# Optimization experiments

Hardware: AMD Instinct MI355X
Metric: run time of the kernel (lower is better)

## Reference

```python
import jax, jax.numpy as jnp
import numpy as np
import math

B, L, D, H = 8, 2048, 1024, 16
DK = D // H
FACTOR = 1
TOP_K = int(FACTOR * math.log(L))  # = 7


def _linear(x, W, b):
    # torch nn.Linear: y = x @ W.T + b, W shape (out, in)
    return x @ W.T + b


def setup_inputs() -> dict:
    rng = jax.random.key(0)
    ks = jax.random.split(rng, 11)
    s = 1.0 / math.sqrt(D)
    inp = {
        "query": jax.random.normal(ks[0], (B, L, D), jnp.float32),
        "key": jax.random.normal(ks[1], (B, L, D), jnp.float32),
        "value": jax.random.normal(ks[2], (B, L, D), jnp.float32),
        "Wq": jax.random.normal(ks[3], (D, D), jnp.float32) * s,
        "bq": jnp.zeros((D,), jnp.float32),
        "Wk": jax.random.normal(ks[4], (D, D), jnp.float32) * s,
        "bk": jnp.zeros((D,), jnp.float32),
        "Wv": jax.random.normal(ks[5], (D, D), jnp.float32) * s,
        "bv": jnp.zeros((D,), jnp.float32),
        "Wo": jax.random.normal(ks[6], (D, D), jnp.float32) * s,
        "bo": jnp.zeros((D,), jnp.float32),
    }
    return inp


def _autocorrelation(q, k, v):
    # q,k,v: (B, H, DK, L)
    q_fft = jnp.fft.rfft(q, axis=-1)
    k_fft = jnp.fft.rfft(k, axis=-1)
    corr = jnp.fft.irfft(q_fft * jnp.conj(k_fft), n=L, axis=-1)  # (B,H,DK,L)

    mean_value = jnp.mean(corr, axis=2)                 # (B,H,L)
    weights, index = jax.lax.top_k(mean_value, TOP_K)   # (B,H,TOP_K)
    tmp_corr = jax.nn.softmax(weights, axis=-1)         # (B,H,TOP_K)

    t = jnp.arange(L)[None, None, :]                    # (1,1,L)
    delays_agg = jnp.zeros_like(v)
    for i in range(TOP_K):  # TOP_K=7, static small loop
        # torch.roll(v, -delay, -1)[..., t] == v[..., (t+delay) % L]
        idx = (t + index[:, :, i:i + 1]) % L            # (B,H,L)
        idx = jnp.broadcast_to(idx[:, :, None, :], v.shape)
        pattern = jnp.take_along_axis(v, idx, axis=-1)  # (B,H,DK,L)
        delays_agg = delays_agg + pattern * tmp_corr[:, :, i][:, :, None, None]
    return delays_agg, tmp_corr


def reference(query, key, value, Wq, bq, Wk, bk, Wv, bv, Wo, bo):
    residual = query
    # project and split heads -> (B, H, DK, L)
    q = _linear(query, Wq, bq).reshape(B, L, H, DK).transpose(0, 2, 3, 1)
    k = _linear(key, Wk, bk).reshape(B, L, H, DK).transpose(0, 2, 3, 1)
    v = _linear(value, Wv, bv).reshape(B, L, H, DK).transpose(0, 2, 3, 1)

    agg, corr_weights = _autocorrelation(q, k, v)       # (B,H,DK,L)
    corr_value = agg.transpose(0, 3, 1, 2).reshape(B, L, D)
    corr_value = _linear(corr_value, Wo, bo)
    # dropout in eval mode = identity
    return corr_value + residual, corr_weights
```

## Files before the change

kernel.cpp:

```cpp
#include <hip/hip_runtime.h>
#include <hip/hip_bf16.h>
#include <math.h>

#define BB   8
#define LL   2048
#define DD   1024
#define HH   16
#define DKK  64
#define TOPK 7

typedef unsigned short u16;
typedef short short8 __attribute__((ext_vector_type(8)));
typedef short s4v    __attribute__((ext_vector_type(4)));
typedef float f32x4  __attribute__((ext_vector_type(4)));
typedef int   int4v  __attribute__((ext_vector_type(4)));
typedef char  char16v __attribute__((ext_vector_type(16)));

#define QT_B    0ull
#define KT_B    67108864ull
#define VBF_B   134217728ull
#define XH_B    167772160ull
#define WH_B    201326592ull
#define WL_B    203423744ull
#define PART_B  201326592ull
#define PART_STRIDE 2064
#define TOPW_B  209780736ull
#define TOPI_B  209784320ull

#define SX_INV  5461.3333f
#define SW_INV  174762.67f
#define CS1     6.8664551e-5f
#define CS2     2.6822090e-7f

__device__ __forceinline__ int2 xcd_swizzle_8x128() {
    const int lin = blockIdx.y * gridDim.x + blockIdx.x;
    const int swz = (lin & 7) * 128 + (lin >> 3);
    return make_int2(swz & 7, swz >> 3);
}

__device__ __forceinline__ u16 f2bf(float f) {
    unsigned u = __float_as_uint(f);
    unsigned r = u + 0x7FFFu + ((u >> 16) & 1u);
    return (u16)(r >> 16);
}
__device__ __forceinline__ float bf2f(u16 h) {
    return __uint_as_float((unsigned)h << 16);
}

__global__ __launch_bounds__(256) void k_split_i8(
    const float* __restrict__ x, char* __restrict__ hi, char* __restrict__ lo,
    float inv_s, int n16)
{
    for (int i = blockIdx.x * 256 + threadIdx.x; i < n16; i += gridDim.x * 256) {
        const float4* xp = (const float4*)(x + (size_t)i * 16);
        float f[16];
        #pragma unroll
        for (int v = 0; v < 4; ++v) {
            float4 t = xp[v];
            f[v*4+0] = t.x; f[v*4+1] = t.y; f[v*4+2] = t.z; f[v*4+3] = t.w;
        }
        char16v h, l;
        #pragma unroll
        for (int j = 0; j < 16; ++j) {
            int q = __float2int_rn(f[j] * inv_s);
            q = min(max(q, -32639), 32639);
            int xl = ((q + 128) & 255) - 128;
            int xh = (q - xl) >> 8;
            h[j] = (char)xh; l[j] = (char)xl;
        }
        *(char16v*)(hi + (size_t)i * 16) = h;
        *(char16v*)(lo + (size_t)i * 16) = l;
    }
}

__global__ __launch_bounds__(256) void k_cvt_bf16(
    const float* __restrict__ x, u16* __restrict__ hi, int n8)
{
    for (int i = blockIdx.x * 256 + threadIdx.x; i < n8; i += gridDim.x * 256) {
        const float4* xp = (const float4*)(x + (size_t)i * 8);
        float4 v0 = xp[0], v1 = xp[1];
        float f[8] = {v0.x, v0.y, v0.z, v0.w, v1.x, v1.y, v1.z, v1.w};
        short8 h8;
        #pragma unroll
        for (int j = 0; j < 8; ++j) h8[j] = (short)f2bf(f[j]);
        *(short8*)(hi + (size_t)i * 8) = h8;
    }
}

__global__ __launch_bounds__(256) void k_transpose_bf(
    const u16* __restrict__ src, u16* __restrict__ dst)
{
    __shared__ u16 tile[32][34];
    const int tx = threadIdx.x & 31, ty = threadIdx.x >> 5;
    const int row0 = blockIdx.y * 32;
    const int col0 = blockIdx.x * 32;
    #pragma unroll
    for (int i = 0; i < 4; ++i)
        tile[ty + i * 8][tx] = src[(size_t)(row0 + ty + i * 8) * 2048 + col0 + tx];
    __syncthreads();
    const int b  = row0 >> 10;
    const int d0 = row0 & 1023;
    #pragma unroll
    for (int i = 0; i < 4; ++i) {
        const int l = col0 + ty + i * 8;
        dst[(size_t)((b << 11) + l) * 1024 + d0 + tx] = tile[tx][ty + i * 8];
    }
}

__device__ __forceinline__ void async16(u16* l, const u16* g) {
    __builtin_amdgcn_global_load_lds(
        (const __attribute__((address_space(1))) void*)g,
        (__attribute__((address_space(3))) void*)l, 16, 0, 0);
}
__device__ __forceinline__ void async16b(char* l, const char* g) {
    __builtin_amdgcn_global_load_lds(
        (const __attribute__((address_space(1))) void*)g,
        (__attribute__((address_space(3))) void*)l, 16, 0, 0);
}

__global__ __launch_bounds__(256, 2) void gemm_i8split(
    const char* __restrict__ Ah, const char* __restrict__ Al,
    const char* __restrict__ Bh, const char* __restrict__ Bl,
    const float* __restrict__ bias, float* __restrict__ outp)
{
    __shared__ __align__(16) char lds[2][4][8192];
    const int t = threadIdx.x;
    const int w = t >> 6, lane = t & 63;
    const int2 tb = xcd_swizzle_8x128();
    const int m0 = tb.y * 128, n0 = tb.x * 128;
    const int srow = lane >> 2, sslot = lane & 3;
    const int r15 = lane & 15, kg = lane >> 4;
    const int wr = w >> 1, wc = w & 1;
    const int r4 = (lane >> 4) * 4;
    const int swzb = (kg ^ (r15 & 3)) << 4;
    const int a_off = (wr * 64 + r15) * 64 + swzb;
    const int b_off = (wc * 64 + r15) * 64 + swzb;

    int4v acc1[4][4], acc2[4][4];
    #pragma unroll
    for (int i = 0; i < 4; ++i)
        #pragma unroll
        for (int j = 0; j < 4; ++j) {
            acc1[i][j] = (int4v){0,0,0,0};
            acc2[i][j] = (int4v){0,0,0,0};
        }

    #define STAGE8(buf, kt)                                                       \
    {                                                                             \
        const int gc0 = (kt) * 64;                                                \
        _Pragma("unroll")                                                         \
        for (int i = 0; i < 2; ++i) {                                             \
            const int row  = w * 32 + i * 16 + srow;                              \
            const int kch  = (sslot ^ (row & 3)) << 4;                            \
            const int loff = w * 2048 + i * 1024;                                 \
            async16b(&lds[buf][0][loff], Ah + (size_t)(m0 + row) * 1024 + gc0 + kch); \
            async16b(&lds[buf][1][loff], Bh + (size_t)(n0 + row) * 1024 + gc0 + kch); \
            async16b(&lds[buf][2][loff], Al + (size_t)(m0 + row) * 1024 + gc0 + kch); \
            async16b(&lds[buf][3][loff], Bl + (size_t)(n0 + row) * 1024 + gc0 + kch); \
        }                                                                         \
    }

    #define COMP8(buf)                                                            \
    {                                                                             \
        const char* cb = &lds[buf][0][0];                                         \
        int4v ah[4], bh4[4], al[4], bl[4];                                        \
        _Pragma("unroll")                                                         \
        for (int mi = 0; mi < 4; ++mi) ah[mi] = *(const int4v*)(cb + a_off + mi * 1024); \
        _Pragma("unroll")                                                         \
        for (int nj = 0; nj < 4; ++nj) bh4[nj] = *(const int4v*)(cb + 8192 + b_off + nj * 1024); \
        _Pragma("unroll")                                                         \
        for (int mi = 0; mi < 4; ++mi)                                            \
            _Pragma("unroll")                                                     \
            for (int nj = 0; nj < 4; ++nj)                                        \
                acc1[mi][nj] = __builtin_amdgcn_mfma_i32_16x16x64_i8(ah[mi], bh4[nj], acc1[mi][nj], 0, 0, 0); \
        _Pragma("unroll")                                                         \
        for (int nj = 0; nj < 4; ++nj) bl[nj] = *(const int4v*)(cb + 24576 + b_off + nj * 1024); \
        _Pragma("unroll")                                                         \
        for (int mi = 0; mi < 4; ++mi)                                            \
            _Pragma("unroll")                                                     \
            for (int nj = 0; nj < 4; ++nj)                                        \
                acc2[mi][nj] = __builtin_amdgcn_mfma_i32_16x16x64_i8(ah[mi], bl[nj], acc2[mi][nj], 0, 0, 0); \
        _Pragma("unroll")                                                         \
        for (int mi = 0; mi < 4; ++mi) al[mi] = *(const int4v*)(cb + 16384 + a_off + mi * 1024); \
        _Pragma("unroll")                                                         \
        for (int mi = 0; mi < 4; ++mi)                                            \
            _Pragma("unroll")                                                     \
            for (int nj = 0; nj < 4; ++nj)                                        \
                acc2[mi][nj] = __builtin_amdgcn_mfma_i32_16x16x64_i8(al[mi], bh4[nj], acc2[mi][nj], 0, 0, 0); \
    }

    STAGE8(0, 0);
    __syncthreads();
    int cur = 0;
    for (int kt = 0; kt < 15; ++kt) {
        STAGE8(cur ^ 1, kt + 1);
        COMP8(cur);
        __syncthreads();
        cur ^= 1;
    }
    COMP8(cur);

    #pragma unroll
    for (int nj = 0; nj < 4; ++nj) {
        const int n = n0 + wc * 64 + nj * 16 + r15;
        const float bs = bias[n];
        #pragma unroll
        for (int mi = 0; mi < 4; ++mi) {
            const int m = m0 + wr * 64 + mi * 16 + r4;
            const int b = m >> 11;
            const int l = m & 2047;
            float4 v;
            v.x = fmaf(CS1, (float)acc1[mi][nj][0], fmaf(CS2, (float)acc2[mi][nj][0], bs));
            v.y = fmaf(CS1, (float)acc1[mi][nj][1], fmaf(CS2, (float)acc2[mi][nj][1], bs));
            v.z = fmaf(CS1, (float)acc1[mi][nj][2], fmaf(CS2, (float)acc2[mi][nj][2], bs));
            v.w = fmaf(CS1, (float)acc1[mi][nj][3], fmaf(CS2, (float)acc2[mi][nj][3], bs));
            *(float4*)(outp + (((size_t)((b << 10) + n)) << 11) + l) = v;
        }
    }
    #undef STAGE8
    #undef COMP8
}

template<int NPROD, int EPI>
__global__ __launch_bounds__(256, 2) void gemm_mfma_bt(
    const u16* __restrict__ Ah, const u16* __restrict__ Al,
    const u16* __restrict__ Bh, const u16* __restrict__ Bl,
    const float* __restrict__ bias, const float* __restrict__ resid,
    float* __restrict__ outp)
{
    constexpr int NARR = (NPROD == 3) ? 4 : 2;
    __shared__ __align__(16) u16 lds[2 * NARR * 4096];
    const int t = threadIdx.x;
    const int w = t >> 6, lane = t & 63;
    const int2 tb = xcd_swizzle_8x128();
    const int m0 = tb.y * 128, n0 = tb.x * 128;
    const int srow = lane >> 2, sslot = lane & 3;
    const int r15 = lane & 15, kg = lane >> 4;
    const int wr = w >> 1, wc = w & 1;
    const int r4 = (lane >> 4) * 4;
    const int swz16 = (kg ^ (r15 & 3)) << 3;
    const int a_off = ((wr * 64 + r15) << 5) + swz16;
    const int b_off = ((wc * 64 + r15) << 5) + swz16;

    f32x4 acc[4][4];
    #pragma unroll
    for (int i = 0; i < 4; ++i)
        #pragma unroll
        for (int j = 0; j < 4; ++j)
            acc[i][j] = (f32x4){0.f, 0.f, 0.f, 0.f};

    #define STAGE(buf, kt)                                                        \
    {                                                                             \
        const int k0s = (kt) * 32;                                                \
        u16* base = &lds[(buf) * NARR * 4096];                                    \
        _Pragma("unroll")                                                         \
        for (int i = 0; i < 2; ++i) {                                             \
            const int row = w * 32 + i * 16 + srow;                               \
            const int kch = ((sslot ^ (row & 3)) << 3);                           \
            const int loff = w * 1024 + i * 512;                                  \
            async16(&base[loff],            Ah + (size_t)(m0 + row) * 1024 + k0s + kch); \
            async16(&base[4096 + loff],     Bh + (size_t)(n0 + row) * 1024 + k0s + kch); \
        }                                                                         \
    }

    #define COMPUTE(buf)                                                          \
    {                                                                             \
        const u16* cb = &lds[(buf) * NARR * 4096];                                \
        short8 ah[4], bh[4];                                                      \
        _Pragma("unroll")                                                         \
        for (int mi = 0; mi < 4; ++mi) ah[mi] = *(const short8*)(cb + a_off + mi * 512); \
        _Pragma("unroll")                                                         \
        for (int nj = 0; nj < 4; ++nj) bh[nj] = *(const short8*)(cb + 4096 + b_off + nj * 512); \
        _Pragma("unroll")                                                         \
        for (int mi = 0; mi < 4; ++mi)                                            \
            _Pragma("unroll")                                                     \
            for (int nj = 0; nj < 4; ++nj)                                        \
                acc[mi][nj] = __builtin_amdgcn_mfma_f32_16x16x32_bf16(ah[mi], bh[nj], acc[mi][nj], 0, 0, 0); \
    }

    STAGE(0, 0);
    __syncthreads();
    int cur = 0;
    for (int kt = 0; kt < 31; ++kt) {
        STAGE(cur ^ 1, kt + 1);
        COMPUTE(cur);
        __syncthreads();
        cur ^= 1;
    }
    COMPUTE(cur);

    if (EPI == 0) {
        #pragma unroll
        for (int nj = 0; nj < 4; ++nj) {
            const int n = n0 + wc * 64 + nj * 16 + r15;
            const float bs = bias[n];
            #pragma unroll
            for (int mi = 0; mi < 4; ++mi) {
                const int m = m0 + wr * 64 + mi * 16 + r4;
                const int b = m >> 11;
                const int l = m & 2047;
                float4 v;
                v.x = acc[mi][nj][0] + bs;
                v.y = acc[mi][nj][1] + bs;
                v.z = acc[mi][nj][2] + bs;
                v.w = acc[mi][nj][3] + bs;
                *(float4*)(outp + (((size_t)((b << 10) + n)) << 11) + l) = v;
            }
        }
    } else if (EPI == 2) {
        u16* outb = (u16*)outp;
        #pragma unroll
        for (int nj = 0; nj < 4; ++nj) {
            const int n = n0 + wc * 64 + nj * 16 + r15;
            const float bs = bias[n];
            #pragma unroll
            for (int mi = 0; mi < 4; ++mi) {
                const int m = m0 + wr * 64 + mi * 16 + r4;
                const int b = m >> 11;
                const int l = m & 2047;
                s4v v;
                #pragma unroll
                for (int r = 0; r < 4; ++r) v[r] = (short)f2bf(acc[mi][nj][r] + bs);
                *(s4v*)(outb + (((size_t)((b << 10) + n)) << 11) + l) = v;
            }
        }
    } else {
        #pragma unroll
        for (int mi = 0; mi < 4; ++mi) {
            #pragma unroll
            for (int r = 0; r < 4; ++r) {
                const int m = m0 + wr * 64 + mi * 16 + r4 + r;
                const float* rrow = resid + ((size_t)m << 10);
                float* orow = outp + ((size_t)m << 10);
                #pragma unroll
                for (int nj = 0; nj < 4; ++nj) {
                    const int n = n0 + wc * 64 + nj * 16 + r15;
                    orow[n] = acc[mi][nj][r] + bias[n] + rrow[n];
                }
            }
        }
    }
    #undef STAGE
    #undef COMPUTE
}

#define IDX(i) ((i) + ((i) >> 3))
#define FFT_BUF 2304

__device__ __forceinline__ float2 c_add(float2 a, float2 b){ return make_float2(a.x+b.x, a.y+b.y); }
__device__ __forceinline__ float2 c_sub(float2 a, float2 b){ return make_float2(a.x-b.x, a.y-b.y); }
__device__ __forceinline__ float2 cmul(float2 a, float2 b){
    return make_float2(fmaf(a.x, b.x, -a.y*b.y), fmaf(a.x, b.y, a.y*b.x));
}
template<bool INV>
__device__ __forceinline__ float2 rot90(float2 z) {
    return INV ? make_float2(-z.y, z.x) : make_float2(z.y, -z.x);
}

template<bool INV>
__device__ __forceinline__ void dft8(const float2* a, float2* y) {
    const float r = 0.70710678118654752f;
    float2 e0 = c_add(a[0], a[4]), e1 = c_sub(a[0], a[4]);
    float2 e2 = c_add(a[2], a[6]), e3 = rot90<INV>(c_sub(a[2], a[6]));
    float2 E0 = c_add(e0, e2), E2 = c_sub(e0, e2);
    float2 E1 = c_add(e1, e3), E3 = c_sub(e1, e3);
    float2 o0 = c_add(a[1], a[5]), o1 = c_sub(a[1], a[5]);
    float2 o2 = c_add(a[3], a[7]), o3 = rot90<INV>(c_sub(a[3], a[7]));
    float2 O0 = c_add(o0, o2), O2 = c_sub(o0, o2);
    float2 O1 = c_add(o1, o3), O3 = c_sub(o1, o3);
    float2 T1 = INV ? make_float2(r*(O1.x - O1.y), r*(O1.x + O1.y))
                    : make_float2(r*(O1.x + O1.y), r*(O1.y - O1.x));
    float2 T2 = rot90<INV>(O2);
    float2 T3 = INV ? make_float2(-r*(O3.x + O3.y), r*(O3.x - O3.y))
                    : make_float2(r*(O3.y - O3.x), -r*(O3.x + O3.y));
    y[0] = c_add(E0, O0); y[4] = c_sub(E0, O0);
    y[1] = c_add(E1, T1); y[5] = c_sub(E1, T1);
    y[2] = c_add(E2, T2); y[6] = c_sub(E2, T2);
    y[3] = c_add(E3, T3); y[7] = c_sub(E3, T3);
}

template<bool INV>
__device__ float2* fft2048_r8(float2* bufA, float2* bufB, const float2* twd, int tid)
{
    float2* src = bufA;
    float2* dst = bufB;
    #pragma unroll
    for (int st = 0; st < 3; ++st) {
        const int s = 1 << (3 * st);
        const int u = tid;
        const int sp = u & ~(s - 1);
        float2 a[8], y[8];
        #pragma unroll
        for (int t = 0; t < 8; ++t) a[t] = src[IDX(u + (t << 8))];
        dft8<INV>(a, y);
        float2 w1 = twd[sp];
        if (INV) w1.y = -w1.y;
        const int ob = u + 7 * sp;
        dst[IDX(ob)]     = y[0];
        dst[IDX(ob + s)] = cmul(y[1], w1);
        float2 w = w1;
        #pragma unroll
        for (int t = 2; t < 8; ++t) {
            w = cmul(w, w1);
            dst[IDX(ob + t * s)] = cmul(y[t], w);
        }
        __syncthreads();
        float2* tmp = src; src = dst; dst = tmp;
    }
    #pragma unroll
    for (int h = 0; h < 2; ++h) {
        const int u = tid + (h << 8);
        float2 a0 = src[IDX(u)],        a1 = src[IDX(u + 512)];
        float2 a2 = src[IDX(u + 1024)], a3 = src[IDX(u + 1536)];
        float2 b0 = c_add(a0, a2), b1 = c_sub(a0, a2);
        float2 b2 = c_add(a1, a3), b3 = rot90<INV>(c_sub(a1, a3));
        dst[IDX(u)]        = c_add(b0, b2);
        dst[IDX(u + 512)]  = c_add(b1, b3);
        dst[IDX(u + 1024)] = c_sub(b0, b2);
        dst[IDX(u + 1536)] = c_sub(b1, b3);
    }
    __syncthreads();
    return dst;
}

__global__ __launch_bounds__(256) void fft_corr_partial(
    const float* __restrict__ qT, const float* __restrict__ kT,
    float* __restrict__ part)
{
    __shared__ float2 bufA[FFT_BUF];
    __shared__ float2 bufB[FFT_BUF];
    __shared__ float2 twd[256];
    const int tid = threadIdx.x;
    const int blk = blockIdx.x;
    const int bh  = blk >> 3, g = blk & 7;
    {
        float s, c;
        sincosf((float)tid * 3.0679615757712823e-3f, &s, &c);
        twd[tid] = make_float2(c, -s);
    }
    float2 racc[4];
    #pragma unroll
    for (int ii = 0; ii < 4; ++ii) racc[ii] = make_float2(0.f, 0.f);
    float2 racc4 = make_float2(0.f, 0.f);

    const float* qbase = qT + ((size_t)bh * DKK + g * 8) * LL;
    const float* kbase = kT + ((size_t)bh * DKK + g * 8) * LL;
    for (int dd = 0; dd < 8; ++dd) {
        __syncthreads();
        const float* qr = qbase + (size_t)dd * LL;
        const float* kr = kbase + (size_t)dd * LL;
        #pragma unroll
        for (int j = 0; j < 8; ++j) {
            const int l = tid + (j << 8);
            bufA[IDX(l)] = make_float2(qr[l], kr[l]);
        }
        __syncthreads();
        float2* res = fft2048_r8<false>(bufA, bufB, twd, tid);
        #pragma unroll
        for (int ii = 0; ii < 4; ++ii) {
            const int f = tid + (ii << 8);
            float2 zf = res[IDX(f)];
            float2 zc = res[IDX((2048 - f) & 2047)];
            float2 Q = make_float2(0.5f*(zf.x + zc.x), 0.5f*(zf.y - zc.y));
            float2 K = make_float2(0.5f*(zf.y + zc.y), -0.5f*(zf.x - zc.x));
            racc[ii].x += Q.x*K.x + Q.y*K.y;
            racc[ii].y += Q.y*K.x - Q.x*K.y;
        }
        if (tid == 0) {
            float2 zf = res[IDX(1024)];
            racc4.x += zf.x * zf.y;
        }
    }
    float* po = part + (size_t)blk * PART_STRIDE;
    #pragma unroll
    for (int ii = 0; ii < 4; ++ii) {
        const int f = tid + (ii << 8);
        po[2*f]     = racc[ii].x;
        po[2*f + 1] = racc[ii].y;
    }
    if (tid == 0) { po[2048] = racc4.x; po[2049] = racc4.y; }
}

__global__ __launch_bounds__(256) void fft_inv_topk(
    const float* __restrict__ part, float* __restrict__ out1,
    float* __restrict__ topw, int* __restrict__ topi)
{
    __shared__ float2 bufA[FFT_BUF];
    __shared__ float2 bufB[FFT_BUF];
    __shared__ float2 twd[256];
    __shared__ float  mv[2048];
    __shared__ float  rv[256];
    __shared__ int    ri[256];
    __shared__ float  selv[TOPK];
    __shared__ int    seli[TOPK];
    const int tid = threadIdx.x;
    const int bh  = blockIdx.x;
    {
        float s, c;
        sincosf((float)tid * 3.0679615757712823e-3f, &s, &c);
        twd[tid] = make_float2(c, -s);
    }
    for (int f = tid; f < 1025; f += 256) {
        float sx = 0.f, sy = 0.f;
        for (int g2 = 0; g2 < 8; ++g2) {
            const float* po = part + (size_t)(bh * 8 + g2) * PART_STRIDE + 2*f;
            sx += po[0]; sy += po[1];
        }
        bufA[IDX(f)] = make_float2(sx, sy);
        if (f > 0 && f < 1024) bufA[IDX(2048 - f)] = make_float2(sx, -sy);
    }
    __syncthreads();
    float2* res = fft2048_r8<true>(bufA, bufB, twd, tid);
    const float scale = 1.0f / (2048.0f * 64.0f);
    #pragma unroll
    for (int j = 0; j < 8; ++j) {
        const int l = tid + (j << 8);
        mv[l] = res[IDX(l)].x * scale;
    }
    __syncthreads();
    for (int it = 0; it < TOPK; ++it) {
        float bvv = -3.0e38f; int bii = 0;
        #pragma unroll
        for (int c = 0; c < 8; ++c) {
            const int idx = tid * 8 + c;
            const float v = mv[idx];
            if (v > bvv) { bvv = v; bii = idx; }
        }
        rv[tid] = bvv; ri[tid] = bii;
        __syncthreads();
        for (int off = 128; off > 0; off >>= 1) {
            if (tid < off) {
                const float v2 = rv[tid + off]; const int i2 = ri[tid + off];
                if (v2 > rv[tid] || (v2 == rv[tid] && i2 < ri[tid])) {
                    rv[tid] = v2; ri[tid] = i2;
                }
            }
            __syncthreads();
        }
        if (tid == 0) { selv[it] = rv[0]; seli[it] = ri[0]; mv[ri[0]] = -3.0e38f; }
        __syncthreads();
    }
    if (tid == 0) {
        const float mx = selv[0];
        float e[TOPK]; float ssum = 0.f;
        #pragma unroll
        for (int i = 0; i < TOPK; ++i) { e[i] = expf(selv[i] - mx); ssum += e[i]; }
        const float inv = 1.0f / ssum;
        #pragma unroll
        for (int i = 0; i < TOPK; ++i) {
            const float w = e[i] * inv;
            out1[bh * TOPK + i] = w;
            topw[bh * TOPK + i] = w;
            topi[bh * TOPK + i] = seli[i];
        }
    }
}

__global__ __launch_bounds__(256) void gather_agg_bf(
    const u16* __restrict__ vbf, const float* __restrict__ topw,
    const int* __restrict__ topi, u16* __restrict__ aggbf)
{
    __shared__ float vrow[2048];
    __shared__ float wv[TOPK];
    __shared__ int   wi[TOPK];
    const int blk = blockIdx.x;
    const int bh  = blk >> 6;
    const int tid = threadIdx.x;
    if (tid < TOPK) {
        wv[tid] = topw[bh * TOPK + tid];
        wi[tid] = topi[bh * TOPK + tid];
    }
    const u16* vr = vbf + (size_t)blk * LL;
    short8 v8 = *(const short8*)(vr + tid * 8);
    #pragma unroll
    for (int j = 0; j < 8; ++j) vrow[tid * 8 + j] = bf2f((u16)v8[j]);
    __syncthreads();
    u16* ar = aggbf + (size_t)blk * LL;
    short8 o8;
    #pragma unroll
    for (int j = 0; j < 8; ++j) {
        const int l = tid * 8 + j;
        float s = 0.f;
        #pragma unroll
        for (int i = 0; i < TOPK; ++i)
            s = fmaf(wv[i], vrow[(l + wi[i]) & 2047], s);
        o8[j] = (short)f2bf(s);
    }
    *(short8*)(ar + tid * 8) = o8;
}

extern "C" void kernel_launch(void* const* d_in, const int* in_sizes, int n_in,
                              void* d_out, int out_size, void* d_ws, size_t ws_size,
                              hipStream_t stream)
{
    const float* query = (const float*)d_in[0];
    const float* key   = (const float*)d_in[1];
    const float* value = (const float*)d_in[2];
    const float* Wq    = (const float*)d_in[3];
    const float* bq    = (const float*)d_in[4];
    const float* Wk    = (const float*)d_in[5];
    const float* bk    = (const float*)d_in[6];
    const float* Wv    = (const float*)d_in[7];
    const float* bv    = (const float*)d_in[8];
    const float* Wo    = (const float*)d_in[9];
    const float* bo    = (const float*)d_in[10];
    float* out = (float*)d_out;
    char*  ws  = (char*)d_ws;

    float* qT    = (float*)(ws + QT_B);
    float* kT    = (float*)(ws + KT_B);
    u16*   vbf   = (u16*)(ws + VBF_B);
    float* part  = (float*)(ws + PART_B);
    float* topw  = (float*)(ws + TOPW_B);
    int*   topi  = (int*)(ws + TOPI_B);
    char* qxh8 = (char*)(ws + KT_B);
    char* qxl8 = (char*)(ws + KT_B + 16777216ull);
    char* qwh8 = (char*)(ws + VBF_B);
    char* qwl8 = (char*)(ws + VBF_B + 1048576ull);
    char* kxh8 = (char*)(ws + VBF_B);
    char* kxl8 = (char*)(ws + VBF_B + 16777216ull);
    char* kwh8 = (char*)(ws + WH_B);
    char* kwl8 = (char*)(ws + WH_B + 1048576ull);
    u16* vxh = (u16*)(ws + XH_B);
    u16* vwh = (u16*)(ws + WH_B);
    u16* aggbf  = (u16*)(ws + XH_B);
    u16* aggrow = (u16*)(ws + VBF_B);
    u16* owh = (u16*)(ws + WH_B);

    const int NX8  = BB * LL * DD / 8;
    const int NW8  = DD * DD / 8;
    const int NX16 = BB * LL * DD / 16;
    const int NW16 = DD * DD / 16;
    dim3 gg(DD / 128, (BB * LL) / 128);

    k_split_i8<<<2048, 256, 0, stream>>>(query, qxh8, qxl8, SX_INV, NX16);
    k_split_i8<<<256, 256, 0, stream>>>(Wq, qwh8, qwl8, SW_INV, NW16);
    gemm_i8split<<<gg, 256, 0, stream>>>(qxh8, qxl8, qwh8, qwl8, bq, qT);
    k_split_i8<<<2048, 256, 0, stream>>>(key, kxh8, kxl8, SX_INV, NX16);
    k_split_i8<<<256, 256, 0, stream>>>(Wk, kwh8, kwl8, SW_INV, NW16);
    gemm_i8split<<<gg, 256, 0, stream>>>(kxh8, kxl8, kwh8, kwl8, bk, kT);
    k_cvt_bf16<<<2048, 256, 0, stream>>>(value, vxh, NX8);
    k_cvt_bf16<<<512, 256, 0, stream>>>(Wv, vwh, NW8);
    gemm_mfma_bt<1, 2><<<gg, 256, 0, stream>>>(vxh, nullptr, vwh, nullptr, bv, nullptr, (float*)vbf);
    fft_corr_partial<<<BB * HH * 8, 256, 0, stream>>>(qT, kT, part);
    fft_inv_topk<<<BB * HH, 256, 0, stream>>>(part, out + 16777216, topw, topi);
    gather_agg_bf<<<BB * HH * DKK, 256, 0, stream>>>(vbf, topw, topi, aggbf);
    k_transpose_bf<<<dim3(64, 256), 256, 0, stream>>>(aggbf, aggrow);
    k_cvt_bf16<<<512, 256, 0, stream>>>(Wo, owh, NW8);
    gemm_mfma_bt<1, 1><<<gg, 256, 0, stream>>>(aggrow, nullptr, owh, nullptr, bo, query, out);
}
```

Measured before the change: 437.3 us.

## Fuse conversion kernels, store Q/K projections as bf16, fuse gather with transpose

The separate fp32-to-int8-split and bf16 conversion launches are merged into one kernel for the activations and one for the weights. The workspace is re-laid out so all buffers coexist. The Q and K int8-split GEMMs now write bf16 instead of fp32, which halves the traffic into the FFT correlation kernel. The gather-aggregate and transpose kernels are fused into one kernel that stages 32 value rows in 128KB of dynamic LDS and writes row-major output directly. The costs are lower precision in the correlation inputs, which can change the top-k delay selection, and a large dynamic LDS allocation on only 256 blocks.

```diff
diff --git a/kernel.cpp b/kernel.cpp
--- a/kernel.cpp
+++ b/kernel.cpp
@@ -16,22 +16,35 @@
 typedef int   int4v  __attribute__((ext_vector_type(4)));
 typedef char  char16v __attribute__((ext_vector_type(16)));
 
-#define QT_B    0ull
-#define KT_B    67108864ull
-#define VBF_B   134217728ull
-#define XH_B    167772160ull
-#define WH_B    201326592ull
-#define WL_B    203423744ull
-#define PART_B  201326592ull
+#define QXH_B   0ull
+#define QXL_B   16777216ull
+#define KXH_B   33554432ull
+#define KXL_B   50331648ull
+#define VXH_B   67108864ull
+#define QWH_B   100663296ull
+#define QWL_B   101711872ull
+#define KWH_B   102760448ull
+#define KWL_B   103809024ull
+#define VWH_B   104857600ull
+#define OWH_B   106954752ull
+#define QTB_B   109051904ull
+#define KTB_B   142606336ull
+#define VBF_B   176160768ull
+#define PART_B  0ull
 #define PART_STRIDE 2064
-#define TOPW_B  209780736ull
-#define TOPI_B  209784320ull
+#define TOPW_B  16777216ull
+#define TOPI_B  16780800ull
 
 #define SX_INV  5461.3333f
 #define SW_INV  174762.67f
 #define CS1     6.8664551e-5f
 #define CS2     2.6822090e-7f
 
+#define NX16 1048576
+#define NW16 65536
+#define NX8  2097152
+#define NW8  131072
+
 __device__ __forceinline__ int2 xcd_swizzle_8x128() {
     const int lin = blockIdx.y * gridDim.x + blockIdx.x;
     const int swz = (lin & 7) * 128 + (lin >> 3);
@@ -47,63 +60,72 @@
     return __uint_as_float((unsigned)h << 16);
 }
 
-__global__ __launch_bounds__(256) void k_split_i8(
-    const float* __restrict__ x, char* __restrict__ hi, char* __restrict__ lo,
-    float inv_s, int n16)
-{
-    for (int i = blockIdx.x * 256 + threadIdx.x; i < n16; i += gridDim.x * 256) {
-        const float4* xp = (const float4*)(x + (size_t)i * 16);
-        float f[16];
-        #pragma unroll
-        for (int v = 0; v < 4; ++v) {
-            float4 t = xp[v];
-            f[v*4+0] = t.x; f[v*4+1] = t.y; f[v*4+2] = t.z; f[v*4+3] = t.w;
-        }
-        char16v h, l;
-        #pragma unroll
-        for (int j = 0; j < 16; ++j) {
-            int q = __float2int_rn(f[j] * inv_s);
-            q = min(max(q, -32639), 32639);
-            int xl = ((q + 128) & 255) - 128;
-            int xh = (q - xl) >> 8;
-            h[j] = (char)xh; l[j] = (char)xl;
-        }
-        *(char16v*)(hi + (size_t)i * 16) = h;
-        *(char16v*)(lo + (size_t)i * 16) = l;
-    }
-}
-
-__global__ __launch_bounds__(256) void k_cvt_bf16(
-    const float* __restrict__ x, u16* __restrict__ hi, int n8)
-{
-    for (int i = blockIdx.x * 256 + threadIdx.x; i < n8; i += gridDim.x * 256) {
-        const float4* xp = (const float4*)(x + (size_t)i * 8);
-        float4 v0 = xp[0], v1 = xp[1];
-        float f[8] = {v0.x, v0.y, v0.z, v0.w, v1.x, v1.y, v1.z, v1.w};
-        short8 h8;
-        #pragma unroll
-        for (int j = 0; j < 8; ++j) h8[j] = (short)f2bf(f[j]);
-        *(short8*)(hi + (size_t)i * 8) = h8;
-    }
-}
-
-__global__ __launch_bounds__(256) void k_transpose_bf(
-    const u16* __restrict__ src, u16* __restrict__ dst)
-{
-    __shared__ u16 tile[32][34];
-    const int tx = threadIdx.x & 31, ty = threadIdx.x >> 5;
-    const int row0 = blockIdx.y * 32;
-    const int col0 = blockIdx.x * 32;
-    #pragma unroll
-    for (int i = 0; i < 4; ++i)
-        tile[ty + i * 8][tx] = src[(size_t)(row0 + ty + i * 8) * 2048 + col0 + tx];
-    __syncthreads();
-    const int b  = row0 >> 10;
-    const int d0 = row0 & 1023;
-    #pragma unroll
-    for (int i = 0; i < 4; ++i) {
-        const int l = col0 + ty + i * 8;
-        dst[(size_t)((b << 11) + l) * 1024 + d0 + tx] = tile[tx][ty + i * 8];
+__device__ __forceinline__ void split16_i8(const float* x, char* hi, char* lo,
+                                           float inv_s, size_t i) {
+    const float4* xp = (const float4*)(x + i * 16);
+    float f[16];
+    #pragma unroll
+    for (int v = 0; v < 4; ++v) {
+        float4 t = xp[v];
+        f[v*4+0] = t.x; f[v*4+1] = t.y; f[v*4+2] = t.z; f[v*4+3] = t.w;
+    }
+    char16v h, l;
+    #pragma unroll
+    for (int j = 0; j < 16; ++j) {
+        int q = __float2int_rn(f[j] * inv_s);
+        q = min(max(q, -32639), 32639);
+        int xl = ((q + 128) & 255) - 128;
+        int xh = (q - xl) >> 8;
+        h[j] = (char)xh; l[j] = (char)xl;
+    }
+    *(char16v*)(hi + i * 16) = h;
+    *(char16v*)(lo + i * 16) = l;
+}
+
+__device__ __forceinline__ void cvt8_bf(const float* x, u16* o, size_t i) {
+    const float4* xp = (const float4*)(x + i * 8);
+    float4 v0 = xp[0], v1 = xp[1];
+    float f[8] = {v0.x, v0.y, v0.z, v0.w, v1.x, v1.y, v1.z, v1.w};
+    short8 h8;
+    #pragma unroll
+    for (int j = 0; j < 8; ++j) h8[j] = (short)f2bf(f[j]);
+    *(short8*)(o + i * 8) = h8;
+}
+
+__global__ __launch_bounds__(256) void k_conv_inputs(
+    const float* __restrict__ q, const float* __restrict__ k,
+    const float* __restrict__ v,
+    char* __restrict__ qh, char* __restrict__ ql,
+    char* __restrict__ kh, char* __restrict__ kl, u16* __restrict__ vx)
+{
+    const int seg  = blockIdx.x >> 11;
+    const int base = (blockIdx.x & 2047) * 256 + threadIdx.x;
+    if (seg == 0) {
+        for (int i = base; i < NX16; i += 524288) split16_i8(q, qh, ql, SX_INV, i);
+    } else if (seg == 1) {
+        for (int i = base; i < NX16; i += 524288) split16_i8(k, kh, kl, SX_INV, i);
+    } else {
+        for (int i = base; i < NX8; i += 524288) cvt8_bf(v, vx, i);
+    }
+}
+
+__global__ __launch_bounds__(256) void k_conv_weights(
+    const float* __restrict__ Wq, const float* __restrict__ Wk,
+    const float* __restrict__ Wv, const float* __restrict__ Wo,
+    char* __restrict__ qwh, char* __restrict__ qwl,
+    char* __restrict__ kwh, char* __restrict__ kwl,
+    u16* __restrict__ vwh, u16* __restrict__ owh)
+{
+    const int seg  = blockIdx.x >> 8;
+    const int base = (blockIdx.x & 255) * 256 + threadIdx.x;
+    if (seg == 0) {
+        split16_i8(Wq, qwh, qwl, SW_INV, base);
+    } else if (seg == 1) {
+        split16_i8(Wk, kwh, kwl, SW_INV, base);
+    } else if (seg == 2) {
+        for (int i = base; i < NW8; i += 65536) cvt8_bf(Wv, vwh, i);
+    } else {
+        for (int i = base; i < NW8; i += 65536) cvt8_bf(Wo, owh, i);
     }
 }
 
@@ -121,7 +143,7 @@
 __global__ __launch_bounds__(256, 2) void gemm_i8split(
     const char* __restrict__ Ah, const char* __restrict__ Al,
     const char* __restrict__ Bh, const char* __restrict__ Bl,
-    const float* __restrict__ bias, float* __restrict__ outp)
+    const float* __restrict__ bias, u16* __restrict__ outb)
 {
     __shared__ __align__(16) char lds[2][4][8192];
     const int t = threadIdx.x;
@@ -209,27 +231,25 @@
             const int m = m0 + wr * 64 + mi * 16 + r4;
             const int b = m >> 11;
             const int l = m & 2047;
-            float4 v;
-            v.x = fmaf(CS1, (float)acc1[mi][nj][0], fmaf(CS2, (float)acc2[mi][nj][0], bs));
-            v.y = fmaf(CS1, (float)acc1[mi][nj][1], fmaf(CS2, (float)acc2[mi][nj][1], bs));
-            v.z = fmaf(CS1, (float)acc1[mi][nj][2], fmaf(CS2, (float)acc2[mi][nj][2], bs));
-            v.w = fmaf(CS1, (float)acc1[mi][nj][3], fmaf(CS2, (float)acc2[mi][nj][3], bs));
-            *(float4*)(outp + (((size_t)((b << 10) + n)) << 11) + l) = v;
+            s4v v;
+            #pragma unroll
+            for (int r = 0; r < 4; ++r)
+                v[r] = (short)f2bf(fmaf(CS1, (float)acc1[mi][nj][r],
+                                   fmaf(CS2, (float)acc2[mi][nj][r], bs)));
+            *(s4v*)(outb + (((size_t)((b << 10) + n)) << 11) + l) = v;
         }
     }
     #undef STAGE8
     #undef COMP8
 }
 
-template<int NPROD, int EPI>
+template<int EPI>
 __global__ __launch_bounds__(256, 2) void gemm_mfma_bt(
-    const u16* __restrict__ Ah, const u16* __restrict__ Al,
-    const u16* __restrict__ Bh, const u16* __restrict__ Bl,
+    const u16* __restrict__ Ah, const u16* __restrict__ Bh,
     const float* __restrict__ bias, const float* __restrict__ resid,
     float* __restrict__ outp)
 {
-    constexpr int NARR = (NPROD == 3) ? 4 : 2;
-    __shared__ __align__(16) u16 lds[2 * NARR * 4096];
+    __shared__ __align__(16) u16 lds[2 * 2 * 4096];
     const int t = threadIdx.x;
     const int w = t >> 6, lane = t & 63;
     const int2 tb = xcd_swizzle_8x128();
@@ -252,20 +272,20 @@
     #define STAGE(buf, kt)                                                        \
     {                                                                             \
         const int k0s = (kt) * 32;                                                \
-        u16* base = &lds[(buf) * NARR * 4096];                                    \
+        u16* base = &lds[(buf) * 2 * 4096];                                       \
         _Pragma("unroll")                                                         \
         for (int i = 0; i < 2; ++i) {                                             \
             const int row = w * 32 + i * 16 + srow;                               \
             const int kch = ((sslot ^ (row & 3)) << 3);                           \
             const int loff = w * 1024 + i * 512;                                  \
-            async16(&base[loff],            Ah + (size_t)(m0 + row) * 1024 + k0s + kch); \
-            async16(&base[4096 + loff],     Bh + (size_t)(n0 + row) * 1024 + k0s + kch); \
+            async16(&base[loff],        Ah + (size_t)(m0 + row) * 1024 + k0s + kch); \
+            async16(&base[4096 + loff], Bh + (size_t)(n0 + row) * 1024 + k0s + kch); \
         }                                                                         \
     }
 
     #define COMPUTE(buf)                                                          \
     {                                                                             \
-        const u16* cb = &lds[(buf) * NARR * 4096];                                \
+        const u16* cb = &lds[(buf) * 2 * 4096];                                   \
         short8 ah[4], bh[4];                                                      \
         _Pragma("unroll")                                                         \
         for (int mi = 0; mi < 4; ++mi) ah[mi] = *(const short8*)(cb + a_off + mi * 512); \
@@ -289,25 +309,7 @@
     }
     COMPUTE(cur);
 
-    if (EPI == 0) {
-        #pragma unroll
-        for (int nj = 0; nj < 4; ++nj) {
-            const int n = n0 + wc * 64 + nj * 16 + r15;
-            const float bs = bias[n];
-            #pragma unroll
-            for (int mi = 0; mi < 4; ++mi) {
-                const int m = m0 + wr * 64 + mi * 16 + r4;
-                const int b = m >> 11;
-                const int l = m & 2047;
-                float4 v;
-                v.x = acc[mi][nj][0] + bs;
-                v.y = acc[mi][nj][1] + bs;
-                v.z = acc[mi][nj][2] + bs;
-                v.w = acc[mi][nj][3] + bs;
-                *(float4*)(outp + (((size_t)((b << 10) + n)) << 11) + l) = v;
-            }
-        }
-    } else if (EPI == 2) {
+    if (EPI == 2) {
         u16* outb = (u16*)outp;
         #pragma unroll
         for (int nj = 0; nj < 4; ++nj) {
@@ -424,7 +426,7 @@
 }
 
 __global__ __launch_bounds__(256) void fft_corr_partial(
-    const float* __restrict__ qT, const float* __restrict__ kT,
+    const u16* __restrict__ qT, const u16* __restrict__ kT,
     float* __restrict__ part)
 {
     __shared__ float2 bufA[FFT_BUF];
@@ -443,17 +445,17 @@
     for (int ii = 0; ii < 4; ++ii) racc[ii] = make_float2(0.f, 0.f);
     float2 racc4 = make_float2(0.f, 0.f);
 
-    const float* qbase = qT + ((size_t)bh * DKK + g * 8) * LL;
-    const float* kbase = kT + ((size_t)bh * DKK + g * 8) * LL;
+    const u16* qbase = qT + ((size_t)bh * DKK + g * 8) * LL;
+    const u16* kbase = kT + ((size_t)bh * DKK + g * 8) * LL;
     for (int dd = 0; dd < 8; ++dd) {
         __syncthreads();
-        const float* qr = qbase + (size_t)dd * LL;
-        const float* kr = kbase + (size_t)dd * LL;
-        #pragma unroll
-        for (int j = 0; j < 8; ++j) {
-            const int l = tid + (j << 8);
-            bufA[IDX(l)] = make_float2(qr[l], kr[l]);
-        }
+        const u16* qr = qbase + (size_t)dd * LL;
+        const u16* kr = kbase + (size_t)dd * LL;
+        short8 q8 = *(const short8*)(qr + tid * 8);
+        short8 k8 = *(const short8*)(kr + tid * 8);
+        #pragma unroll
+        for (int j = 0; j < 8; ++j)
+            bufA[IDX(tid * 8 + j)] = make_float2(bf2f((u16)q8[j]), bf2f((u16)k8[j]));
         __syncthreads();
         float2* res = fft2048_r8<false>(bufA, bufB, twd, tid);
         #pragma unroll
@@ -556,37 +558,44 @@
     }
 }
 
-__global__ __launch_bounds__(256) void gather_agg_bf(
+__global__ __launch_bounds__(256) void gather_tr(
     const u16* __restrict__ vbf, const float* __restrict__ topw,
-    const int* __restrict__ topi, u16* __restrict__ aggbf)
-{
-    __shared__ float vrow[2048];
+    const int* __restrict__ topi, u16* __restrict__ aggrow)
+{
+    extern __shared__ u16 vstage[];
     __shared__ float wv[TOPK];
     __shared__ int   wi[TOPK];
-    const int blk = blockIdx.x;
-    const int bh  = blk >> 6;
-    const int tid = threadIdx.x;
+    const int blk  = blockIdx.x;
+    const int bh   = blk >> 1, half = blk & 1;
+    const int b    = bh >> 4, h = bh & 15;
+    const int tid  = threadIdx.x;
     if (tid < TOPK) {
         wv[tid] = topw[bh * TOPK + tid];
         wi[tid] = topi[bh * TOPK + tid];
     }
-    const u16* vr = vbf + (size_t)blk * LL;
-    short8 v8 = *(const short8*)(vr + tid * 8);
-    #pragma unroll
-    for (int j = 0; j < 8; ++j) vrow[tid * 8 + j] = bf2f((u16)v8[j]);
+    const u16* vsrc = vbf + ((size_t)bh * DKK + half * 32) * LL;
+    short8* vs8 = (short8*)vstage;
+    #pragma unroll
+    for (int k = 0; k < 32; ++k)
+        vs8[tid + k * 256] = *(const short8*)(vsrc + (size_t)(tid + k * 256) * 8);
     __syncthreads();
-    u16* ar = aggbf + (size_t)blk * LL;
-    short8 o8;
-    #pragma unroll
-    for (int j = 0; j < 8; ++j) {
-        const int l = tid * 8 + j;
-        float s = 0.f;
-        #pragma unroll
-        for (int i = 0; i < TOPK; ++i)
-            s = fmaf(wv[i], vrow[(l + wi[i]) & 2047], s);
-        o8[j] = (short)f2bf(s);
-    }
-    *(short8*)(ar + tid * 8) = o8;
+    const int doff = h * 64 + half * 32;
+    for (int c = 0; c < 8; ++c) {
+        const int l = c * 256 + tid;
+        u16* orow = aggrow + ((size_t)((b << 11) + l) << 10) + doff;
+        short8 o[4];
+        #pragma unroll
+        for (int d = 0; d < 32; ++d) {
+            float s = 0.f;
+            #pragma unroll
+            for (int i = 0; i < TOPK; ++i)
+                s = fmaf(wv[i], bf2f(vstage[d * 2048 + ((l + wi[i]) & 2047)]), s);
+            o[d >> 3][d & 7] = (short)f2bf(s);
+        }
+        #pragma unroll
+        for (int q = 0; q < 4; ++q)
+            *(short8*)(orow + q * 8) = o[q];
+    }
 }
 
 extern "C" void kernel_launch(void* const* d_in, const int* in_sizes, int n_in,
@@ -607,45 +616,36 @@
     float* out = (float*)d_out;
     char*  ws  = (char*)d_ws;
 
-    float* qT    = (float*)(ws + QT_B);
-    float* kT    = (float*)(ws + KT_B);
-    u16*   vbf   = (u16*)(ws + VBF_B);
-    float* part  = (float*)(ws + PART_B);
-    float* topw  = (float*)(ws + TOPW_B);
-    int*   topi  = (int*)(ws + TOPI_B);
-    char* qxh8 = (char*)(ws + KT_B);
-    char* qxl8 = (char*)(ws + KT_B + 16777216ull);
-    char* qwh8 = (char*)(ws + VBF_B);
-    char* qwl8 = (char*)(ws + VBF_B + 1048576ull);
-    char* kxh8 = (char*)(ws + VBF_B);
-    char* kxl8 = (char*)(ws + VBF_B + 16777216ull);
-    char* kwh8 = (char*)(ws + WH_B);
-    char* kwl8 = (char*)(ws + WH_B + 1048576ull);
-    u16* vxh = (u16*)(ws + XH_B);
-    u16* vwh = (u16*)(ws + WH_B);
-    u16* aggbf  = (u16*)(ws + XH_B);
-    u16* aggrow = (u16*)(ws + VBF_B);
-    u16* owh = (u16*)(ws + WH_B);
-
-    const int NX8  = BB * LL * DD / 8;
-    const int NW8  = DD * DD / 8;
-    const int NX16 = BB * LL * DD / 16;
-    const int NW16 = DD * DD / 16;
+    char* qxh = (char*)(ws + QXH_B);
+    char* qxl = (char*)(ws + QXL_B);
+    char* kxh = (char*)(ws + KXH_B);
+    char* kxl = (char*)(ws + KXL_B);
+    u16*  vxh = (u16*)(ws + VXH_B);
+    char* qwh = (char*)(ws + QWH_B);
+    char* qwl = (char*)(ws + QWL_B);
+    char* kwh = (char*)(ws + KWH_B);
+    char* kwl = (char*)(ws + KWL_B);
+    u16*  vwh = (u16*)(ws + VWH_B);
+    u16*  owh = (u16*)(ws + OWH_B);
+    u16*  qTb = (u16*)(ws + QTB_B);
+    u16*  kTb = (u16*)(ws + KTB_B);
+    u16*  vbf = (u16*)(ws + VBF_B);
+    float* part = (float*)(ws + PART_B);
+    float* topw = (float*)(ws + TOPW_B);
+    int*   topi = (int*)(ws + TOPI_B);
+    u16*  aggrow = (u16*)(ws + QTB_B);
+
     dim3 gg(DD / 128, (BB * LL) / 128);
 
-    k_split_i8<<<2048, 256, 0, stream>>>(query, qxh8, qxl8, SX_INV, NX16);
-    k_split_i8<<<256, 256, 0, stream>>>(Wq, qwh8, qwl8, SW_INV, NW16);
-    gemm_i8split<<<gg, 256, 0, stream>>>(qxh8, qxl8, qwh8, qwl8, bq, qT);
-    k_split_i8<<<2048, 256, 0, stream>>>(key, kxh8, kxl8, SX_INV, NX16);
-    k_split_i8<<<256, 256, 0, stream>>>(Wk, kwh8, kwl8, SW_INV, NW16);
-    gemm_i8split<<<gg, 256, 0, stream>>>(kxh8, kxl8, kwh8, kwl8, bk, kT);
-    k_cvt_bf16<<<2048, 256, 0, stream>>>(value, vxh, NX8);
-    k_cvt_bf16<<<512, 256, 0, stream>>>(Wv, vwh, NW8);
-    gemm_mfma_bt<1, 2><<<gg, 256, 0, stream>>>(vxh, nullptr, vwh, nullptr, bv, nullptr, (float*)vbf);
-    fft_corr_partial<<<BB * HH * 8, 256, 0, stream>>>(qT, kT, part);
+    k_conv_inputs<<<6144, 256, 0, stream>>>(query, key, value,
+                                            qxh, qxl, kxh, kxl, vxh);
+    k_conv_weights<<<1024, 256, 0, stream>>>(Wq, Wk, Wv, Wo,
+                                             qwh, qwl, kwh, kwl, vwh, owh);
+    gemm_i8split<<<gg, 256, 0, stream>>>(qxh, qxl, qwh, qwl, bq, qTb);
+    gemm_i8split<<<gg, 256, 0, stream>>>(kxh, kxl, kwh, kwl, bk, kTb);
+    gemm_mfma_bt<2><<<gg, 256, 0, stream>>>(vxh, vwh, bv, nullptr, (float*)vbf);
+    fft_corr_partial<<<BB * HH * 8, 256, 0, stream>>>(qTb, kTb, part);
     fft_inv_topk<<<BB * HH, 256, 0, stream>>>(part, out + 16777216, topw, topi);
-    gather_agg_bf<<<BB * HH * DKK, 256, 0, stream>>>(vbf, topw, topi, aggbf);
-    k_transpose_bf<<<dim3(64, 256), 256, 0, stream>>>(aggbf, aggrow);
-    k_cvt_bf16<<<512, 256, 0, stream>>>(Wo, owh, NW8);
-    gemm_mfma_bt<1, 1><<<gg, 256, 0, stream>>>(aggrow, nullptr, owh, nullptr, bo, query, out);
-}
+    gather_tr<<<BB * HH * 2, 256, 131072, stream>>>(vbf, topw, topi, aggrow);
+    gemm_mfma_bt<1><<<gg, 256, 0, stream>>>(aggrow, owh, bo, query, out);
+}
```

After: 388.7 us. 1.13x faster.
